# Kernel optimization log

Measured on AMD Instinct MI355X. Metric: run time of the kernel, lower is better.

Reference implementation:

```python
import jax, jax.numpy as jnp
import numpy as np

DIM = 1024
HIDDEN = 1024
NUM_EXPERTS = 8
TOP_K = 2


def setup_inputs() -> dict:
    key = jax.random.key(0)
    ks = jax.random.split(key, 8)
    std = 0.02
    x = jax.random.normal(ks[0], (2, 1024, DIM), dtype=jnp.float32)
    gate_w = jax.random.normal(ks[1], (NUM_EXPERTS, DIM), dtype=jnp.float32) * std
    w1 = jax.random.normal(ks[2], (NUM_EXPERTS, DIM, HIDDEN), dtype=jnp.float32) * std
    w2 = jax.random.normal(ks[3], (NUM_EXPERTS, HIDDEN, DIM), dtype=jnp.float32) * std
    w3 = jax.random.normal(ks[4], (NUM_EXPERTS, DIM, HIDDEN), dtype=jnp.float32) * std
    w1s = jax.random.normal(ks[5], (1, DIM, HIDDEN), dtype=jnp.float32) * std
    w2s = jax.random.normal(ks[6], (1, HIDDEN, DIM), dtype=jnp.float32) * std
    w3s = jax.random.normal(ks[7], (1, DIM, HIDDEN), dtype=jnp.float32) * std
    return {"x": x, "gate_w": gate_w, "w1": w1, "w2": w2, "w3": w3,
            "w1s": w1s, "w2s": w2s, "w3s": w3s}


def reference(x, gate_w, w1, w2, w3, w1s, w2s, w3s):
    bs, slen, dim = x.shape
    xt = x.reshape(bs * slen, dim)                       # [N, d]

    # ---- token-choice top-k router (softmax in fp32) ----
    logits = xt @ gate_w.T                               # [N, E]
    scores = jax.nn.softmax(logits.astype(jnp.float32), axis=1).astype(x.dtype)
    top_scores, sel = jax.lax.top_k(scores, TOP_K)       # [N, K]
    sel_flat = sel.reshape(-1)                           # [N*K]
    order = jnp.argsort(sel_flat, stable=True)           # sort tokens by expert
    top_scores_sorted = top_scores.reshape(-1)[order]    # [T]
    token_idx = order // TOP_K                           # [T] source token per routed row
    eid = sel_flat[order]                                # [T] expert id per routed row

    # ---- dispatch: gather + pre-scale by router score ----
    routed_in = xt[token_idx] * top_scores_sorted[:, None]   # [T, d]

    # ---- grouped SwiGLU experts (fixed loop over experts, masked) ----
    out_routed = jnp.zeros_like(routed_in)
    for e in range(NUM_EXPERTS):
        m = (eid == e)[:, None]
        xe = jnp.where(m, routed_in, 0.0)
        h = jax.nn.silu(xe @ w1[e]) * (xe @ w3[e])
        out_routed = out_routed + jnp.where(m, h @ w2[e], 0.0)

    # ---- shared expert over all tokens ----
    hs = jax.nn.silu(xt @ w1s[0]) * (xt @ w3s[0])
    out = hs @ w2s[0]                                    # [N, d]

    # ---- combine: scatter-add routed outputs ----
    out = out.at[token_idx].add(out_routed)
    return out.reshape(bs, slen, dim)
```

## Files before the change

### kernel.cpp

```cpp
#include <hip/hip_runtime.h>
#include <hip/hip_bf16.h>


#define DIM 1024
#define NTOK 2048
#define NEXP 8
#define NENT 4096
#define ROWS_CAP 8192
#define MAX_TILES 64
#define MM (DIM * DIM)

typedef float f32x4 __attribute__((ext_vector_type(4)));
typedef __bf16 bf16x8 __attribute__((ext_vector_type(8)));

__device__ __forceinline__ unsigned short f2bf(float f) {
  unsigned int u = __builtin_bit_cast(unsigned int, f);
  unsigned int r = u + 0x7FFFu + ((u >> 16) & 1u);
  return (unsigned short)(r >> 16);
}
__device__ __forceinline__ float bf2f(unsigned short h) {
  unsigned int u = ((unsigned int)h) << 16;
  return __builtin_bit_cast(float, u);
}
__device__ __forceinline__ void gload_lds16(const unsigned short* g, unsigned short* l) {
  __builtin_amdgcn_global_load_lds((__attribute__((address_space(1))) const void*)g,
                                   (__attribute__((address_space(3))) void*)l, 16, 0, 0);
}

__device__ __forceinline__ void brick_transpose(const float* __restrict__ src,
                                                unsigned short* __restrict__ dst,
                                                int n_blk, int k_blk,
                                                unsigned short* lds) {
  int c0 = n_blk * 128, r0 = k_blk * 128;
  int tid = threadIdx.x;
  int q = tid & 31;
  int kq0 = tid >> 5;

  const float* sp0 = src + (size_t)(r0 + kq0 * 4) * DIM + c0 + q * 4;
  const float* sp1 = sp0 + (size_t)64 * DIM;
  float4 v0 = *(const float4*)(sp0 + 0 * DIM);
  float4 v1 = *(const float4*)(sp0 + 1 * DIM);
  float4 v2 = *(const float4*)(sp0 + 2 * DIM);
  float4 v3 = *(const float4*)(sp0 + 3 * DIM);
  float4 v4 = *(const float4*)(sp1 + 0 * DIM);
  float4 v5 = *(const float4*)(sp1 + 1 * DIM);
  float4 v6 = *(const float4*)(sp1 + 2 * DIM);
  float4 v7 = *(const float4*)(sp1 + 3 * DIM);
  {
    float a0[4] = {v0.x, v0.y, v0.z, v0.w};
    float a1[4] = {v1.x, v1.y, v1.z, v1.w};
    float a2[4] = {v2.x, v2.y, v2.z, v2.w};
    float a3[4] = {v3.x, v3.y, v3.z, v3.w};
    float b0[4] = {v4.x, v4.y, v4.z, v4.w};
    float b1[4] = {v5.x, v5.y, v5.z, v5.w};
    float b2[4] = {v6.x, v6.y, v6.z, v6.w};
    float b3[4] = {v7.x, v7.y, v7.z, v7.w};
#pragma unroll
    for (int j = 0; j < 4; j++) {
      int row = q * 4 + j;
      {
        int kq = kq0;
        int ch = kq >> 1, half = kq & 1;
        unsigned int off = (unsigned int)row * 128 + ((ch ^ (row & 15)) * 8 + half * 4);
        uint2 p;
        p.x = f2bf(a0[j]) | ((unsigned int)f2bf(a1[j]) << 16);
        p.y = f2bf(a2[j]) | ((unsigned int)f2bf(a3[j]) << 16);
        *(uint2*)(lds + off) = p;
      }
      {
        int kq = kq0 + 16;
        int ch = kq >> 1, half = kq & 1;
        unsigned int off = (unsigned int)row * 128 + ((ch ^ (row & 15)) * 8 + half * 4);
        uint2 p;
        p.x = f2bf(b0[j]) | ((unsigned int)f2bf(b1[j]) << 16);
        p.y = f2bf(b2[j]) | ((unsigned int)f2bf(b3[j]) << 16);
        *(uint2*)(lds + off) = p;
      }
    }
  }
  __syncthreads();

  size_t bbase = ((size_t)n_blk * 32 + (size_t)k_blk * 4) * 4096;
#pragma unroll
  for (int i = 0; i < 4; i++) {
    int g = tid + i * 512;
    int kcr = g >> 9;
    int c = g & 511;
    int row = c >> 2, p = c & 3;
    int koff = (p - (row >> 1)) & 3;
    int ch = kcr * 4 + koff;
    uint4 val = *(const uint4*)(lds + (unsigned int)row * 128 + (ch ^ (row & 15)) * 8);
    *(uint4*)(dst + bbase + (size_t)g * 8) = val;
  }
}

__global__ __launch_bounds__(512) void t13_router(
    const float* __restrict__ x, const float* __restrict__ gw,
    const float* __restrict__ w1, const float* __restrict__ w3,
    const float* __restrict__ w1s, const float* __restrict__ w3s,
    unsigned short* __restrict__ w1t, unsigned short* __restrict__ w3t,
    unsigned short* __restrict__ w1st, unsigned short* __restrict__ w3st,
    unsigned short* __restrict__ xbf,
    int* __restrict__ e0, int* __restrict__ e1,
    float* __restrict__ s0, float* __restrict__ s1) {
  __shared__ __align__(16) unsigned short lds[128 * 128];
  int b = blockIdx.x;
  if (b < 256) {
    int lane = threadIdx.x & 63;
    int t = b * 8 + (threadIdx.x >> 6);
    const float4* xr4 = (const float4*)(x + (size_t)t * DIM);
    float4 xv[4];
#pragma unroll
    for (int i = 0; i < 4; i++) xv[i] = xr4[i * 64 + lane];

    ushort4* xb4 = (ushort4*)(xbf + (size_t)t * DIM);
#pragma unroll
    for (int i = 0; i < 4; i++) {
      ushort4 o;
      o.x = f2bf(xv[i].x); o.y = f2bf(xv[i].y); o.z = f2bf(xv[i].z); o.w = f2bf(xv[i].w);
      xb4[i * 64 + lane] = o;
    }
    if (t == 0) {
      ushort4 zz; zz.x = zz.y = zz.z = zz.w = 0;
      ushort4* pb4 = (ushort4*)(xbf + (size_t)NTOK * DIM);
#pragma unroll
      for (int i = 0; i < 4; i++) pb4[i * 64 + lane] = zz;
    }

    float acc[NEXP];
#pragma unroll
    for (int e = 0; e < NEXP; e++) {
      const float4* g4 = (const float4*)(gw + (size_t)e * DIM);
      float a = 0.f;
#pragma unroll
      for (int i = 0; i < 4; i++) {
        float4 g = g4[i * 64 + lane];
        a += xv[i].x * g.x + xv[i].y * g.y + xv[i].z * g.z + xv[i].w * g.w;
      }
      acc[e] = a;
    }
#pragma unroll
    for (int e = 0; e < NEXP; e++) {
      float v = acc[e];
      for (int o = 32; o > 0; o >>= 1) v += __shfl_xor(v, o);
      acc[e] = v;
    }
    if (lane == 0) {
      float m = acc[0];
#pragma unroll
      for (int e = 1; e < NEXP; e++) m = fmaxf(m, acc[e]);
      float ex[NEXP]; float Z = 0.f;
#pragma unroll
      for (int e = 0; e < NEXP; e++) { ex[e] = __expf(acc[e] - m); Z += ex[e]; }
      float inv = 1.f / Z;
      float sc[NEXP];
#pragma unroll
      for (int e = 0; e < NEXP; e++) sc[e] = ex[e] * inv;
      int b0 = 0; float v0 = sc[0];
#pragma unroll
      for (int e = 1; e < NEXP; e++) if (sc[e] > v0) { v0 = sc[e]; b0 = e; }
      int b1 = -1; float v1 = -1.f;
#pragma unroll
      for (int e = 0; e < NEXP; e++) if (e != b0 && sc[e] > v1) { v1 = sc[e]; b1 = e; }
      e0[t] = b0; e1[t] = b1; s0[t] = v0; s1[t] = v1;
    }
  } else {
    int bb = b - 256;
    int slice = bb >> 6, s6 = bb & 63;
    int n_blk = s6 & 7, k_blk = s6 >> 3;
    const float* src; unsigned short* dst;
    if (slice < 8)       { src = w1 + (size_t)slice * MM;       dst = w1t + (size_t)slice * MM; }
    else if (slice < 16) { src = w3 + (size_t)(slice - 8) * MM; dst = w3t + (size_t)(slice - 8) * MM; }
    else if (slice == 16){ src = w1s; dst = w1st; }
    else                 { src = w3s; dst = w3st; }
    brick_transpose(src, dst, n_blk, k_blk, lds);
  }
}

__global__ __launch_bounds__(256) void build_groups(
    const int* __restrict__ e0, const int* __restrict__ e1,
    const float* __restrict__ s0, const float* __restrict__ s1,
    int* __restrict__ gtok, float* __restrict__ gsc, int* __restrict__ row_of,
    int* __restrict__ tile_e, int* __restrict__ tile_r0, int* __restrict__ ntiles,
    int* __restrict__ base8out) {
  __shared__ unsigned int wsum[4][4];
  __shared__ int offl[256][NEXP];
  __shared__ int lrl[256][NEXP];
  int t = threadIdx.x, lane = t & 63, wave = t >> 6;

  for (int i = t; i < ROWS_CAP; i += 256) { gtok[i] = NTOK; gsc[i] = 0.f; }

  unsigned int pc[4] = {0, 0, 0, 0};
#pragma unroll
  for (int i = 0; i < 16; i++) {
    int ent = t * 16 + i;
    int tok = ent >> 1;
    int e = (ent & 1) ? e1[tok] : e0[tok];
    unsigned int add = 1u << ((e & 1) * 16);
    int c = e >> 1;
    if (c == 0) pc[0] += add; else if (c == 1) pc[1] += add;
    else if (c == 2) pc[2] += add; else pc[3] += add;
  }
  unsigned int incl[4] = {pc[0], pc[1], pc[2], pc[3]};
#pragma unroll
  for (int o = 1; o < 64; o <<= 1) {
    unsigned int u0 = __shfl_up(incl[0], o), u1 = __shfl_up(incl[1], o);
    unsigned int u2 = __shfl_up(incl[2], o), u3 = __shfl_up(incl[3], o);
    if (lane >= o) { incl[0] += u0; incl[1] += u1; incl[2] += u2; incl[3] += u3; }
  }
  if (lane == 63) { wsum[wave][0] = incl[0]; wsum[wave][1] = incl[1];
                    wsum[wave][2] = incl[2]; wsum[wave][3] = incl[3]; }
  __syncthreads();
  unsigned int T[4], pre[4] = {0, 0, 0, 0};
#pragma unroll
  for (int c = 0; c < 4; c++)
    T[c] = wsum[0][c] + wsum[1][c] + wsum[2][c] + wsum[3][c];
#pragma unroll
  for (int w = 0; w < 3; w++)
    if (wave > w) { pre[0] += wsum[w][0]; pre[1] += wsum[w][1];
                    pre[2] += wsum[w][2]; pre[3] += wsum[w][3]; }
  int base[NEXP + 1];
  {
    int b = 0;
#pragma unroll
    for (int e = 0; e < NEXP; e++) {
      int tot = (int)((T[e >> 1] >> ((e & 1) * 16)) & 0xFFFFu);
      base[e] = b; b += (tot + 127) & ~127;
    }
    base[NEXP] = b;
  }
#pragma unroll
  for (int e = 0; e < NEXP; e++) {
    unsigned int ex = (incl[e >> 1] + pre[e >> 1] - pc[e >> 1]);
    offl[t][e] = (int)((ex >> ((e & 1) * 16)) & 0xFFFFu);
    lrl[t][e] = 0;
  }
  if (t == 0) {
    int nt = 0;
#pragma unroll
    for (int e = 0; e < NEXP; e++) {
      int tot = (int)((T[e >> 1] >> ((e & 1) * 16)) & 0xFFFFu);
      int ntl = (tot + 127) >> 7;
      for (int i = 0; i < ntl; i++) { tile_e[nt] = e; tile_r0[nt] = base[e] + i * 128; nt++; }
    }
    for (int i = 0; i < NTOK / 128; i++) { tile_e[nt] = NEXP; tile_r0[nt] = base[NEXP] + i * 128; nt++; }
    *ntiles = nt;
    *base8out = base[NEXP];
  }
  __syncthreads();

#pragma unroll
  for (int i = 0; i < 16; i++) {
    int ent = t * 16 + i;
    int tok = ent >> 1;
    int k = ent & 1;
    int e = k ? e1[tok] : e0[tok];
    float s = k ? s1[tok] : s0[tok];
    int pos = base[e] + offl[t][e] + lrl[t][e];
    lrl[t][e]++;
    gtok[pos] = tok; gsc[pos] = s; row_of[ent] = pos;
  }
  for (int i = t; i < NTOK; i += 256) { gtok[base[NEXP] + i] = i; gsc[base[NEXP] + i] = 1.0f; }
}

__global__ __launch_bounds__(512, 4) void gemm13_t2(
    const unsigned short* __restrict__ xbf,
    const unsigned short* __restrict__ W1, const unsigned short* __restrict__ W1s,
    const unsigned short* __restrict__ W3, const unsigned short* __restrict__ W3s,
    const float* __restrict__ w2, const float* __restrict__ w2s,
    unsigned short* __restrict__ w2t, unsigned short* __restrict__ w2st,
    unsigned short* __restrict__ H,
    const int* __restrict__ gtok, const float* __restrict__ gsc,
    const int* __restrict__ tile_e, const int* __restrict__ tile_r0,
    const int* __restrict__ ntiles) {
  __shared__ __align__(16) char smem[49664];
  int b = blockIdx.x;
  if (b >= 512) {
    int bb = b - 512;
    int slice = bb >> 6, s6 = bb & 63;
    int n_blk = s6 & 7, k_blk = s6 >> 3;
    const float* src; unsigned short* dst;
    if (slice < 8) { src = w2 + (size_t)slice * MM; dst = w2t + (size_t)slice * MM; }
    else           { src = w2s; dst = w2st; }
    brick_transpose(src, dst, n_blk, k_blk, (unsigned short*)smem);
    return;
  }
  int ti = b >> 3;
  if (ti >= *ntiles) return;
  int e = tile_e[ti];
  int row0 = tile_r0[ti];
  int col0 = (b & 7) * 128;
  const unsigned short* B1 = (e < NEXP) ? (W1 + (size_t)e * MM) : W1s;
  const unsigned short* B3 = (e < NEXP) ? (W3 + (size_t)e * MM) : W3s;

  unsigned short* As  = (unsigned short*)smem;
  unsigned short* Bs1 = (unsigned short*)(smem + 16384);
  unsigned short* Bs3 = (unsigned short*)(smem + 32768);
  float* ss = (float*)(smem + 49152);

  int tid = threadIdx.x;
  int wave = tid >> 6, lane = tid & 63;
  int wrow = (wave >> 2) * 64, wcol = (wave & 3) * 32;

  if (tid < 128) ss[tid] = gsc[row0 + tid];

  f32x4 acc1[4][2], acc3[4][2];
#pragma unroll
  for (int m = 0; m < 4; m++)
#pragma unroll
    for (int n = 0; n < 2; n++) { acc1[m][n] = f32x4{0.f,0.f,0.f,0.f}; acc3[m][n] = f32x4{0.f,0.f,0.f,0.f}; }

  int arow = tid >> 2;
  int akoff = (((tid & 3) - (arow >> 1)) & 3) * 8;
  const unsigned short* ga  = xbf + (size_t)gtok[row0 + arow] * DIM + akoff;
  const unsigned short* gb1 = B1 + ((size_t)(col0 >> 7) * 32) * 4096 + (size_t)tid * 8;
  const unsigned short* gb3 = B3 + ((size_t)(col0 >> 7) * 32) * 4096 + (size_t)tid * 8;
  unsigned short* lA  = As  + wave * 512;
  unsigned short* lB1 = Bs1 + wave * 512;
  unsigned short* lB3 = Bs3 + wave * 512;

  int kc = lane >> 4, rl = lane & 15;

  for (int it = 0; it < 16; it++) {
    int k0 = it * 64;
    size_t boff = (size_t)(it * 2) * 4096;
    gload_lds16(ga + k0,      lA);
    gload_lds16(ga + k0 + 32, lA + 4096);
    gload_lds16(gb1 + boff,        lB1);
    gload_lds16(gb1 + boff + 4096, lB1 + 4096);
    gload_lds16(gb3 + boff,        lB3);
    gload_lds16(gb3 + boff + 4096, lB3 + 4096);
    __syncthreads();

#pragma unroll
    for (int h = 0; h < 2; h++) {
      const bf16x8* Ap  = (const bf16x8*)As  + h * 512;
      const bf16x8* B1p = (const bf16x8*)Bs1 + h * 512;
      const bf16x8* B3p = (const bf16x8*)Bs3 + h * 512;
      bf16x8 af[4], b1f[2], b3f[2];
#pragma unroll
      for (int m = 0; m < 4; m++) {
        int row = wrow + m * 16 + rl;
        af[m] = Ap[row * 4 + ((kc + (row >> 1)) & 3)];
      }
#pragma unroll
      for (int n = 0; n < 2; n++) {
        int row = wcol + n * 16 + rl;
        int p = row * 4 + ((kc + (row >> 1)) & 3);
        b1f[n] = B1p[p];
        b3f[n] = B3p[p];
      }
#pragma unroll
      for (int m = 0; m < 4; m++)
#pragma unroll
        for (int n = 0; n < 2; n++) {
          acc1[m][n] = __builtin_amdgcn_mfma_f32_16x16x32_bf16(af[m], b1f[n], acc1[m][n], 0, 0, 0);
          acc3[m][n] = __builtin_amdgcn_mfma_f32_16x16x32_bf16(af[m], b3f[n], acc3[m][n], 0, 0, 0);
        }
    }
    __syncthreads();
  }

  int rj = lane >> 4, cl = lane & 15;
#pragma unroll
  for (int m = 0; m < 4; m++)
#pragma unroll
    for (int n = 0; n < 2; n++)
#pragma unroll
      for (int j = 0; j < 4; j++) {
        int lr = wrow + m * 16 + rj * 4 + j;
        float s = ss[lr];
        float a = s * acc1[m][n][j];
        float g = s * acc3[m][n][j];
        float si = a / (1.f + __expf(-a));
        H[(size_t)(row0 + lr) * DIM + (col0 + wcol + n * 16 + cl)] = f2bf(si * g);
      }
}

__global__ __launch_bounds__(512, 4) void gemm2(
    const unsigned short* __restrict__ A, const unsigned short* __restrict__ W,
    const unsigned short* __restrict__ Wsh, unsigned short* __restrict__ C,
    const int* __restrict__ tile_e, const int* __restrict__ tile_r0,
    const int* __restrict__ ntiles) {
  if ((int)blockIdx.y >= *ntiles) return;
  int e = tile_e[blockIdx.y];
  int row0 = tile_r0[blockIdx.y];
  int col0 = blockIdx.x * 128;
  const unsigned short* B = (e < NEXP) ? (W + (size_t)e * MM) : Wsh;

  __shared__ __align__(16) unsigned short As[2 * 4096];
  __shared__ __align__(16) unsigned short Bs[2 * 4096];

  int tid = threadIdx.x;
  int wave = tid >> 6, lane = tid & 63;
  int wrow = (wave & 3) * 32, wcol = (wave >> 2) * 64;

  f32x4 acc[2][4];
#pragma unroll
  for (int m = 0; m < 2; m++)
#pragma unroll
    for (int n = 0; n < 4; n++) acc[m][n] = f32x4{0.f, 0.f, 0.f, 0.f};

  int arow = tid >> 2;
  int akoff = (((tid & 3) - (arow >> 1)) & 3) * 8;
  const unsigned short* ga = A + (size_t)(row0 + arow) * DIM + akoff;
  const unsigned short* gb = B + ((size_t)(col0 >> 7) * 32) * 4096 + (size_t)tid * 8;
  unsigned short* lA = As + wave * 512;
  unsigned short* lB = Bs + wave * 512;

  int kc = lane >> 4, rl = lane & 15;

  for (int it = 0; it < 16; it++) {
    int k0 = it * 64;
    size_t boff = (size_t)(it * 2) * 4096;
    gload_lds16(ga + k0,      lA);
    gload_lds16(ga + k0 + 32, lA + 4096);
    gload_lds16(gb + boff,        lB);
    gload_lds16(gb + boff + 4096, lB + 4096);
    __syncthreads();

#pragma unroll
    for (int h = 0; h < 2; h++) {
      const bf16x8* Ap = (const bf16x8*)As + h * 512;
      const bf16x8* Bp = (const bf16x8*)Bs + h * 512;
      bf16x8 af[2], bfr[4];
#pragma unroll
      for (int m = 0; m < 2; m++) {
        int row = wrow + m * 16 + rl;
        af[m] = Ap[row * 4 + ((kc + (row >> 1)) & 3)];
      }
#pragma unroll
      for (int n = 0; n < 4; n++) {
        int row = wcol + n * 16 + rl;
        bfr[n] = Bp[row * 4 + ((kc + (row >> 1)) & 3)];
      }
#pragma unroll
      for (int m = 0; m < 2; m++)
#pragma unroll
        for (int n = 0; n < 4; n++)
          acc[m][n] = __builtin_amdgcn_mfma_f32_16x16x32_bf16(af[m], bfr[n], acc[m][n], 0, 0, 0);
    }
    __syncthreads();
  }

  int rj = lane >> 4, cl = lane & 15;
#pragma unroll
  for (int m = 0; m < 2; m++)
#pragma unroll
    for (int n = 0; n < 4; n++)
#pragma unroll
      for (int j = 0; j < 4; j++) {
        int r = row0 + wrow + m * 16 + rj * 4 + j;
        int c = col0 + wcol + n * 16 + cl;
        C[(size_t)r * DIM + c] = f2bf(acc[m][n][j]);
      }
}

__global__ __launch_bounds__(256) void combine(const unsigned short* __restrict__ routb,
                                               const int* __restrict__ row_of,
                                               const int* __restrict__ base8,
                                               float* __restrict__ out) {
  int t = blockIdx.x;
  int c = threadIdx.x * 4;
  int r0 = row_of[2 * t], r1 = row_of[2 * t + 1];
  int rs = *base8 + t;
  ushort4 v0 = *(const ushort4*)(routb + (size_t)r0 * DIM + c);
  ushort4 v1 = *(const ushort4*)(routb + (size_t)r1 * DIM + c);
  ushort4 v2 = *(const ushort4*)(routb + (size_t)rs * DIM + c);
  float4 o;
  o.x = bf2f(v0.x) + bf2f(v1.x) + bf2f(v2.x);
  o.y = bf2f(v0.y) + bf2f(v1.y) + bf2f(v2.y);
  o.z = bf2f(v0.z) + bf2f(v1.z) + bf2f(v2.z);
  o.w = bf2f(v0.w) + bf2f(v1.w) + bf2f(v2.w);
  *(float4*)(out + (size_t)t * DIM + c) = o;
}

extern "C" void kernel_launch(void* const* d_in, const int* in_sizes, int n_in,
                              void* d_out, int out_size, void* d_ws, size_t ws_size,
                              hipStream_t stream) {
  const float* x   = (const float*)d_in[0];
  const float* gw  = (const float*)d_in[1];
  const float* w1  = (const float*)d_in[2];
  const float* w2  = (const float*)d_in[3];
  const float* w3  = (const float*)d_in[4];
  const float* w1s = (const float*)d_in[5];
  const float* w2s = (const float*)d_in[6];
  const float* w3s = (const float*)d_in[7];
  float* out = (float*)d_out;
  char* ws = (char*)d_ws;

  const size_t MB = 1ull << 20;
  unsigned short* w1t  = (unsigned short*)(ws + 0 * MB);
  unsigned short* w3t  = (unsigned short*)(ws + 16 * MB);
  unsigned short* w2t  = (unsigned short*)(ws + 32 * MB);
  unsigned short* w1st = (unsigned short*)(ws + 48 * MB);
  unsigned short* w3st = (unsigned short*)(ws + 50 * MB);
  unsigned short* w2st = (unsigned short*)(ws + 52 * MB);
  unsigned short* xbf  = (unsigned short*)(ws + 54 * MB);
  unsigned short* hbuf = (unsigned short*)(ws + 60 * MB);
  unsigned short* routb= (unsigned short*)(ws + 76 * MB);
  char* meta = ws + 108 * MB;
  int*   e0p    = (int*)meta;
  int*   e1p    = e0p + NTOK;
  float* s0p    = (float*)(e1p + NTOK);
  float* s1p    = s0p + NTOK;
  int*   gtok   = (int*)(s1p + NTOK);
  float* gsc    = (float*)(gtok + ROWS_CAP);
  int*   row_of = (int*)(gsc + ROWS_CAP);
  int*   tile_e = row_of + NENT;
  int*   tile_r0= tile_e + MAX_TILES;
  int*   ntiles = tile_r0 + MAX_TILES;
  int*   base8  = ntiles + 1;

  t13_router<<<256 + 18 * 64, 512, 0, stream>>>(
      x, gw, w1, w3, w1s, w3s, w1t, w3t, w1st, w3st, xbf, e0p, e1p, s0p, s1p);
  build_groups<<<1, 256, 0, stream>>>(e0p, e1p, s0p, s1p, gtok, gsc, row_of,
                                      tile_e, tile_r0, ntiles, base8);
  gemm13_t2<<<512 + 9 * 64, 512, 0, stream>>>(
      xbf, w1t, w1st, w3t, w3st, w2, w2s, w2t, w2st, hbuf,
      gtok, gsc, tile_e, tile_r0, ntiles);
  dim3 gg(8, MAX_TILES);
  gemm2<<<gg, 512, 0, stream>>>(hbuf, w2t, w2st, routb, tile_e, tile_r0, ntiles);
  combine<<<NTOK, 256, 0, stream>>>(routb, row_of, base8, out);
}
```

Baseline: 95.78 us.

## Double-buffer LDS loads in expert GEMMs with vmcnt-based prefetch pipeline

Both expert GEMM kernels now split K into 32 steps of 32 and use two LDS buffers. Loads for step it+2 are issued while step it is being computed, and a partial s_waitcnt vmcnt waits only for the current buffer. The goal is to hide global-to-LDS load latency that the old load-then-sync loop exposed. The cost is reliance on hand-counted vmcnt values and raw barriers, which is fragile if the compiler reorders or adds memory ops. Each step also does half the MFMA work, which shrinks the compute available to cover a barrier.

```diff
diff --git a/kernel.cpp b/kernel.cpp
--- a/kernel.cpp
+++ b/kernel.cpp
@@ -321,22 +321,22 @@
 
   int kc = lane >> 4, rl = lane & 15;
 
-  for (int it = 0; it < 16; it++) {
-    int k0 = it * 64;
-    size_t boff = (size_t)(it * 2) * 4096;
-    gload_lds16(ga + k0,      lA);
-    gload_lds16(ga + k0 + 32, lA + 4096);
-    gload_lds16(gb1 + boff,        lB1);
-    gload_lds16(gb1 + boff + 4096, lB1 + 4096);
-    gload_lds16(gb3 + boff,        lB3);
-    gload_lds16(gb3 + boff + 4096, lB3 + 4096);
-    __syncthreads();
-
-#pragma unroll
-    for (int h = 0; h < 2; h++) {
-      const bf16x8* Ap  = (const bf16x8*)As  + h * 512;
-      const bf16x8* B1p = (const bf16x8*)Bs1 + h * 512;
-      const bf16x8* B3p = (const bf16x8*)Bs3 + h * 512;
+#define STAGE13(P, IT)                                         \
+  { gload_lds16(ga + (IT) * 32, lA + (P) * 4096);              \
+    gload_lds16(gb1 + (size_t)(IT) * 4096, lB1 + (P) * 4096);  \
+    gload_lds16(gb3 + (size_t)(IT) * 4096, lB3 + (P) * 4096); }
+
+  STAGE13(0, 0);
+  STAGE13(1, 1);
+  for (int it = 0; it < 32; it++) {
+    int p = it & 1;
+    if (it < 31) asm volatile("s_waitcnt vmcnt(3)" ::: "memory");
+    else         asm volatile("s_waitcnt vmcnt(0)" ::: "memory");
+    __builtin_amdgcn_s_barrier();
+    {
+      const bf16x8* Ap  = (const bf16x8*)(As  + p * 4096);
+      const bf16x8* B1p = (const bf16x8*)(Bs1 + p * 4096);
+      const bf16x8* B3p = (const bf16x8*)(Bs3 + p * 4096);
       bf16x8 af[4], b1f[2], b3f[2];
 #pragma unroll
       for (int m = 0; m < 4; m++) {
@@ -346,9 +346,9 @@
 #pragma unroll
       for (int n = 0; n < 2; n++) {
         int row = wcol + n * 16 + rl;
-        int p = row * 4 + ((kc + (row >> 1)) & 3);
-        b1f[n] = B1p[p];
-        b3f[n] = B3p[p];
+        int pp = row * 4 + ((kc + (row >> 1)) & 3);
+        b1f[n] = B1p[pp];
+        b3f[n] = B3p[pp];
       }
 #pragma unroll
       for (int m = 0; m < 4; m++)
@@ -358,7 +358,9 @@
           acc3[m][n] = __builtin_amdgcn_mfma_f32_16x16x32_bf16(af[m], b3f[n], acc3[m][n], 0, 0, 0);
         }
     }
-    __syncthreads();
+    __builtin_amdgcn_s_barrier();
+    asm volatile("" ::: "memory");
+    if (it + 2 < 32) STAGE13(p, it + 2);
   }
 
   int rj = lane >> 4, cl = lane & 15;
@@ -410,19 +412,20 @@
 
   int kc = lane >> 4, rl = lane & 15;
 
-  for (int it = 0; it < 16; it++) {
-    int k0 = it * 64;
-    size_t boff = (size_t)(it * 2) * 4096;
-    gload_lds16(ga + k0,      lA);
-    gload_lds16(ga + k0 + 32, lA + 4096);
-    gload_lds16(gb + boff,        lB);
-    gload_lds16(gb + boff + 4096, lB + 4096);
-    __syncthreads();
-
-#pragma unroll
-    for (int h = 0; h < 2; h++) {
-      const bf16x8* Ap = (const bf16x8*)As + h * 512;
-      const bf16x8* Bp = (const bf16x8*)Bs + h * 512;
+#define STAGE2(P, IT)                                        \
+  { gload_lds16(ga + (IT) * 32, lA + (P) * 4096);            \
+    gload_lds16(gb + (size_t)(IT) * 4096, lB + (P) * 4096); }
+
+  STAGE2(0, 0);
+  STAGE2(1, 1);
+  for (int it = 0; it < 32; it++) {
+    int p = it & 1;
+    if (it < 31) asm volatile("s_waitcnt vmcnt(2)" ::: "memory");
+    else         asm volatile("s_waitcnt vmcnt(0)" ::: "memory");
+    __builtin_amdgcn_s_barrier();
+    {
+      const bf16x8* Ap = (const bf16x8*)(As + p * 4096);
+      const bf16x8* Bp = (const bf16x8*)(Bs + p * 4096);
       bf16x8 af[2], bfr[4];
 #pragma unroll
       for (int m = 0; m < 2; m++) {
@@ -440,7 +443,9 @@
         for (int n = 0; n < 4; n++)
           acc[m][n] = __builtin_amdgcn_mfma_f32_16x16x32_bf16(af[m], bfr[n], acc[m][n], 0, 0, 0);
     }
-    __syncthreads();
+    __builtin_amdgcn_s_barrier();
+    asm volatile("" ::: "memory");
+    if (it + 2 < 32) STAGE2(p, it + 2);
   }
 
   int rj = lane >> 4, cl = lane & 15;
```

After: 99.21 us. 1.04x slower.

## Move part of weight transpose into group-building kernel and raise MFMA priority

Applied to the files above, without the earlier changes.

Three expert slices of the w1 bf16 transpose move out of the router kernel into the single-block build_groups kernel, which becomes build_t. It runs with extra blocks so the serial grouping work overlaps with useful transpose work instead of leaving the GPU mostly idle. The grouping block now uses 512 threads with only 256 active in the scan. The gemm13 inner loop also wraps its MFMA sequence in s_setprio to favour the math wavefronts over loads.

```diff
diff --git a/kernel.cpp b/kernel.cpp
--- a/kernel.cpp
+++ b/kernel.cpp
@@ -169,37 +169,52 @@
     int slice = bb >> 6, s6 = bb & 63;
     int n_blk = s6 & 7, k_blk = s6 >> 3;
     const float* src; unsigned short* dst;
-    if (slice < 8)       { src = w1 + (size_t)slice * MM;       dst = w1t + (size_t)slice * MM; }
-    else if (slice < 16) { src = w3 + (size_t)(slice - 8) * MM; dst = w3t + (size_t)(slice - 8) * MM; }
-    else if (slice == 16){ src = w1s; dst = w1st; }
+    if (slice < 5)       { src = w1 + (size_t)(slice + 3) * MM; dst = w1t + (size_t)(slice + 3) * MM; }
+    else if (slice < 13) { src = w3 + (size_t)(slice - 5) * MM; dst = w3t + (size_t)(slice - 5) * MM; }
+    else if (slice == 13){ src = w1s; dst = w1st; }
     else                 { src = w3s; dst = w3st; }
     brick_transpose(src, dst, n_blk, k_blk, lds);
   }
 }
 
-__global__ __launch_bounds__(256) void build_groups(
+__global__ __launch_bounds__(512) void build_t(
     const int* __restrict__ e0, const int* __restrict__ e1,
     const float* __restrict__ s0, const float* __restrict__ s1,
+    const float* __restrict__ w1, unsigned short* __restrict__ w1t,
     int* __restrict__ gtok, float* __restrict__ gsc, int* __restrict__ row_of,
     int* __restrict__ tile_e, int* __restrict__ tile_r0, int* __restrict__ ntiles,
     int* __restrict__ base8out) {
+  __shared__ __align__(16) unsigned short lds[128 * 128];
   __shared__ unsigned int wsum[4][4];
   __shared__ int offl[256][NEXP];
   __shared__ int lrl[256][NEXP];
+
+  int b = blockIdx.x;
+  if (b > 0) {
+    int bb = b - 1;
+    int slice = bb >> 6, s6 = bb & 63;
+    brick_transpose(w1 + (size_t)slice * MM, w1t + (size_t)slice * MM,
+                    s6 & 7, s6 >> 3, lds);
+    return;
+  }
+
   int t = threadIdx.x, lane = t & 63, wave = t >> 6;
-
-  for (int i = t; i < ROWS_CAP; i += 256) { gtok[i] = NTOK; gsc[i] = 0.f; }
+  bool act = t < 256;
+
+  for (int i = t; i < ROWS_CAP; i += 512) { gtok[i] = NTOK; gsc[i] = 0.f; }
 
   unsigned int pc[4] = {0, 0, 0, 0};
-#pragma unroll
-  for (int i = 0; i < 16; i++) {
-    int ent = t * 16 + i;
-    int tok = ent >> 1;
-    int e = (ent & 1) ? e1[tok] : e0[tok];
-    unsigned int add = 1u << ((e & 1) * 16);
-    int c = e >> 1;
-    if (c == 0) pc[0] += add; else if (c == 1) pc[1] += add;
-    else if (c == 2) pc[2] += add; else pc[3] += add;
+  if (act) {
+#pragma unroll
+    for (int i = 0; i < 16; i++) {
+      int ent = t * 16 + i;
+      int tok = ent >> 1;
+      int e = (ent & 1) ? e1[tok] : e0[tok];
+      unsigned int add = 1u << ((e & 1) * 16);
+      int c = e >> 1;
+      if (c == 0) pc[0] += add; else if (c == 1) pc[1] += add;
+      else if (c == 2) pc[2] += add; else pc[3] += add;
+    }
   }
   unsigned int incl[4] = {pc[0], pc[1], pc[2], pc[3]};
 #pragma unroll
@@ -208,8 +223,8 @@
     unsigned int u2 = __shfl_up(incl[2], o), u3 = __shfl_up(incl[3], o);
     if (lane >= o) { incl[0] += u0; incl[1] += u1; incl[2] += u2; incl[3] += u3; }
   }
-  if (lane == 63) { wsum[wave][0] = incl[0]; wsum[wave][1] = incl[1];
-                    wsum[wave][2] = incl[2]; wsum[wave][3] = incl[3]; }
+  if (act && lane == 63) { wsum[wave][0] = incl[0]; wsum[wave][1] = incl[1];
+                           wsum[wave][2] = incl[2]; wsum[wave][3] = incl[3]; }
   __syncthreads();
   unsigned int T[4], pre[4] = {0, 0, 0, 0};
 #pragma unroll
@@ -221,19 +236,21 @@
                     pre[2] += wsum[w][2]; pre[3] += wsum[w][3]; }
   int base[NEXP + 1];
   {
-    int b = 0;
+    int bsum = 0;
 #pragma unroll
     for (int e = 0; e < NEXP; e++) {
       int tot = (int)((T[e >> 1] >> ((e & 1) * 16)) & 0xFFFFu);
-      base[e] = b; b += (tot + 127) & ~127;
-    }
-    base[NEXP] = b;
-  }
-#pragma unroll
-  for (int e = 0; e < NEXP; e++) {
-    unsigned int ex = (incl[e >> 1] + pre[e >> 1] - pc[e >> 1]);
-    offl[t][e] = (int)((ex >> ((e & 1) * 16)) & 0xFFFFu);
-    lrl[t][e] = 0;
+      base[e] = bsum; bsum += (tot + 127) & ~127;
+    }
+    base[NEXP] = bsum;
+  }
+  if (act) {
+#pragma unroll
+    for (int e = 0; e < NEXP; e++) {
+      unsigned int ex = (incl[e >> 1] + pre[e >> 1] - pc[e >> 1]);
+      offl[t][e] = (int)((ex >> ((e & 1) * 16)) & 0xFFFFu);
+      lrl[t][e] = 0;
+    }
   }
   if (t == 0) {
     int nt = 0;
@@ -249,18 +266,20 @@
   }
   __syncthreads();
 
-#pragma unroll
-  for (int i = 0; i < 16; i++) {
-    int ent = t * 16 + i;
-    int tok = ent >> 1;
-    int k = ent & 1;
-    int e = k ? e1[tok] : e0[tok];
-    float s = k ? s1[tok] : s0[tok];
-    int pos = base[e] + offl[t][e] + lrl[t][e];
-    lrl[t][e]++;
-    gtok[pos] = tok; gsc[pos] = s; row_of[ent] = pos;
-  }
-  for (int i = t; i < NTOK; i += 256) { gtok[base[NEXP] + i] = i; gsc[base[NEXP] + i] = 1.0f; }
+  if (act) {
+#pragma unroll
+    for (int i = 0; i < 16; i++) {
+      int ent = t * 16 + i;
+      int tok = ent >> 1;
+      int k = ent & 1;
+      int e = k ? e1[tok] : e0[tok];
+      float s = k ? s1[tok] : s0[tok];
+      int pos = base[e] + offl[t][e] + lrl[t][e];
+      lrl[t][e]++;
+      gtok[pos] = tok; gsc[pos] = s; row_of[ent] = pos;
+    }
+  }
+  for (int i = t; i < NTOK; i += 512) { gtok[base[NEXP] + i] = i; gsc[base[NEXP] + i] = 1.0f; }
 }
 
 __global__ __launch_bounds__(512, 4) void gemm13_t2(
@@ -350,6 +369,7 @@
         b1f[n] = B1p[p];
         b3f[n] = B3p[p];
       }
+      __builtin_amdgcn_s_setprio(1);
 #pragma unroll
       for (int m = 0; m < 4; m++)
 #pragma unroll
@@ -357,6 +377,7 @@
           acc1[m][n] = __builtin_amdgcn_mfma_f32_16x16x32_bf16(af[m], b1f[n], acc1[m][n], 0, 0, 0);
           acc3[m][n] = __builtin_amdgcn_mfma_f32_16x16x32_bf16(af[m], b3f[n], acc3[m][n], 0, 0, 0);
         }
+      __builtin_amdgcn_s_setprio(0);
     }
     __syncthreads();
   }
@@ -512,10 +533,10 @@
   int*   ntiles = tile_r0 + MAX_TILES;
   int*   base8  = ntiles + 1;
 
-  t13_router<<<256 + 18 * 64, 512, 0, stream>>>(
+  t13_router<<<256 + 15 * 64, 512, 0, stream>>>(
       x, gw, w1, w3, w1s, w3s, w1t, w3t, w1st, w3st, xbf, e0p, e1p, s0p, s1p);
-  build_groups<<<1, 256, 0, stream>>>(e0p, e1p, s0p, s1p, gtok, gsc, row_of,
-                                      tile_e, tile_r0, ntiles, base8);
+  build_t<<<1 + 3 * 64, 512, 0, stream>>>(e0p, e1p, s0p, s1p, w1, w1t,
+                                          gtok, gsc, row_of, tile_e, tile_r0, ntiles, base8);
   gemm13_t2<<<512 + 9 * 64, 512, 0, stream>>>(
       xbf, w1t, w1st, w3t, w3st, w2, w2s, w2t, w2st, hbuf,
       gtok, gsc, tile_e, tile_r0, ntiles);
```

Result: no change. 94.31 us (-1.5%).
